# Kernel tuning notes

Hardware: AMD Instinct MI355X
Metric: run time of the kernel (lower is better)

## Reference

```python
import jax, jax.numpy as jnp
import numpy as np

S = 3072        # total tokens (3 images x 1024 patches)
E = 1280        # n_embed
H = 16          # n_heads
HD = E // H     # head_dim = 80
NSEG = 3


def rotate_half(x):
    x1 = x[..., : x.shape[-1] // 2]
    x2 = x[..., x.shape[-1] // 2 :]
    return jnp.concatenate((-x2, x1), axis=-1)


def setup_inputs() -> dict:
    key = jax.random.key(0)
    ks = jax.random.split(key, 6)
    x = jax.random.normal(ks[0], (S, E), dtype=jnp.float32)
    rotary_pos_emb = jax.random.normal(ks[1], (S, HD // 2), dtype=jnp.float32)
    qkv_w = jax.random.normal(ks[2], (3 * E, E), dtype=jnp.float32) * 0.02
    qkv_b = jax.random.normal(ks[3], (3 * E,), dtype=jnp.float32) * 0.02
    proj_w = jax.random.normal(ks[4], (E, E), dtype=jnp.float32) * 0.02
    proj_b = jax.random.normal(ks[5], (E,), dtype=jnp.float32) * 0.02
    cu_seqlens = (jnp.arange(NSEG + 1, dtype=jnp.int32) * (S // NSEG))  # [0,1024,2048,3072]
    return {"x": x, "rotary_pos_emb": rotary_pos_emb, "qkv_w": qkv_w,
            "qkv_b": qkv_b, "proj_w": proj_w, "proj_b": proj_b,
            "cu_seqlens": cu_seqlens}


def reference(x, rotary_pos_emb, qkv_w, qkv_b, proj_w, proj_b, cu_seqlens):
    seq_len = x.shape[0]
    # qkv projection (torch Linear: x @ W.T + b)
    qkv = (x @ qkv_w.T + qkv_b).reshape(seq_len, 3, H, HD)
    q, k, v = qkv[:, 0], qkv[:, 1], qkv[:, 2]          # each [S, H, HD]

    # inline RoPE: cos/sin repeated over the two halves of head_dim
    cos = jnp.cos(rotary_pos_emb)
    sin = jnp.sin(rotary_pos_emb)
    cos = jnp.concatenate([cos, cos], axis=-1)[:, None, :]  # [S, 1, HD]
    sin = jnp.concatenate([sin, sin], axis=-1)[:, None, :]
    q = q * cos + rotate_half(q) * sin
    k = k * cos + rotate_half(k) * sin

    # block-diagonal segment mask from cu_seqlens
    seg = jnp.searchsorted(cu_seqlens, jnp.arange(seq_len), side="right")  # [S]
    mask = seg[:, None] == seg[None, :]                 # [S, S] bool

    scale = jnp.asarray(1.0 / np.sqrt(HD), dtype=q.dtype)
    scores = jnp.einsum("qhd,khd->hqk", q, k) * scale   # [H, S, S]
    scores = jnp.where(mask[None], scores, jnp.finfo(scores.dtype).min)
    attn = jax.nn.softmax(scores, axis=-1)
    out = jnp.einsum("hqk,khd->qhd", attn, v).reshape(seq_len, E)
    return out @ proj_w.T + proj_b
```

## Files before the change

kernel.cpp:

```cpp
#include <hip/hip_runtime.h>
#include <hip/hip_bf16.h>
#include <math.h>

#define SEQ   3072
#define EMB   1280
#define NHEAD 16
#define HDIM  80
#define QKVN  3840
#define NSEGS 3

typedef __attribute__((ext_vector_type(8))) short bf16x8;
typedef __attribute__((ext_vector_type(4))) short bf16x4;
typedef __attribute__((ext_vector_type(4))) float f32x4;

__device__ __forceinline__ short f2bf(float f) {
    __hip_bfloat16 h = __float2bfloat16(f);
    return *reinterpret_cast<short*>(&h);
}
__device__ __forceinline__ float bf2f(short s) {
    unsigned int u = ((unsigned int)(unsigned short)s) << 16;
    union { unsigned int u; float f; } c; c.u = u;
    return c.f;
}

__device__ __forceinline__ void gload_lds16(const void* g, void* l) {
    __builtin_amdgcn_global_load_lds(
        (const __attribute__((address_space(1))) unsigned int*)g,
        (__attribute__((address_space(3))) unsigned int*)l, 16, 0, 0);
}

__global__ __launch_bounds__(256)
void cvt_bf16_kernel(const float* __restrict__ in, short* __restrict__ out, int n8)
{
    int i = blockIdx.x * 256 + threadIdx.x;
    if (i >= n8) return;
    float4 a = *reinterpret_cast<const float4*>(&in[i*8]);
    float4 b = *reinterpret_cast<const float4*>(&in[i*8+4]);
    bf16x8 o;
    o[0]=f2bf(a.x); o[1]=f2bf(a.y); o[2]=f2bf(a.z); o[3]=f2bf(a.w);
    o[4]=f2bf(b.x); o[5]=f2bf(b.y); o[6]=f2bf(b.z); o[7]=f2bf(b.w);
    *reinterpret_cast<bf16x8*>(&out[i*8]) = o;
}

__device__ __forceinline__ void store_val(float v, float* p) { *p = v; }
__device__ __forceinline__ void store_val(float v, short* p) { *p = f2bf(v); }

template<typename OT>
__global__ __launch_bounds__(256)
void gemm_bf16_nt(const short* __restrict__ A, int lda,
                  const short* __restrict__ B,
                  const float* __restrict__ bias, OT* __restrict__ C,
                  int M, int N, int K)
{
    __shared__ short As[128][32];
    __shared__ short Bs[128][32];

    const int tid = threadIdx.x;
    const int w   = tid >> 6;
    const int l   = tid & 63;
    const int l15 = l & 15;
    const int l4  = l >> 4;
    const int wr  = w >> 1;
    const int wc  = w & 1;
    const int row0 = blockIdx.y * 128;
    const int col0 = blockIdx.x * 128;

    const int srow = l >> 2;
    const int sk   = (l & 3) * 8;

    f32x4 acc[4][4];
    #pragma unroll
    for (int mi = 0; mi < 4; ++mi)
        #pragma unroll
        for (int ni = 0; ni < 4; ++ni) acc[mi][ni] = (f32x4){0.f,0.f,0.f,0.f};

    for (int k0 = 0; k0 < K; k0 += 32) {
        {
            const int c0 = w, c1 = w + 4;
            gload_lds16(&A[(size_t)(row0 + c0*16 + srow) * lda + k0 + sk], &As[c0*16][0]);
            gload_lds16(&A[(size_t)(row0 + c1*16 + srow) * lda + k0 + sk], &As[c1*16][0]);
            gload_lds16(&B[(size_t)(col0 + c0*16 + srow) * K   + k0 + sk], &Bs[c0*16][0]);
            gload_lds16(&B[(size_t)(col0 + c1*16 + srow) * K   + k0 + sk], &Bs[c1*16][0]);
        }
        __syncthreads();

        bf16x8 af[4], bfr[4];
        #pragma unroll
        for (int mi = 0; mi < 4; ++mi)
            af[mi] = *reinterpret_cast<const bf16x8*>(&As[wr*64 + mi*16 + l15][l4*8]);
        #pragma unroll
        for (int ni = 0; ni < 4; ++ni)
            bfr[ni] = *reinterpret_cast<const bf16x8*>(&Bs[wc*64 + ni*16 + l15][l4*8]);

        #pragma unroll
        for (int mi = 0; mi < 4; ++mi)
            #pragma unroll
            for (int ni = 0; ni < 4; ++ni)
                acc[mi][ni] = __builtin_amdgcn_mfma_f32_16x16x32_bf16(
                    af[mi], bfr[ni], acc[mi][ni], 0, 0, 0);
        __syncthreads();
    }

    #pragma unroll
    for (int ni = 0; ni < 4; ++ni) {
        int col = col0 + wc*64 + ni*16 + l15;
        float bv = bias[col];
        #pragma unroll
        for (int mi = 0; mi < 4; ++mi) {
            #pragma unroll
            for (int r = 0; r < 4; ++r) {
                size_t row = (size_t)(row0 + wr*64 + mi*16 + l4*4 + r);
                store_val(acc[mi][ni][r] + bv, &C[row * (size_t)N + col]);
            }
        }
    }
}

__global__ __launch_bounds__(256)
void rope_bf16_kernel(short* __restrict__ qkv, const float* __restrict__ rpe)
{
    int idx = blockIdx.x * 256 + threadIdx.x;
    int blk = idx % 5;
    int h   = (idx / 5) % NHEAD;
    int s   = (idx / (5*NHEAD)) % SEQ;
    int t   = idx / (5*NHEAD*SEQ);
    int d0  = blk * 8;

    const float* rp = rpe + s*40 + d0;
    short* p = qkv + (size_t)s*QKVN + t*EMB + h*HDIM + d0;
    bf16x8 v0 = *reinterpret_cast<const bf16x8*>(p);
    bf16x8 v1 = *reinterpret_cast<const bf16x8*>(p + 40);
    bf16x8 o0, o1;
    #pragma unroll
    for (int j = 0; j < 8; ++j) {
        float ang = rp[j];
        float sn = sinf(ang), cs = cosf(ang);
        float a = bf2f(v0[j]), b = bf2f(v1[j]);
        o0[j] = f2bf(a*cs - b*sn);
        o1[j] = f2bf(b*cs + a*sn);
    }
    *reinterpret_cast<bf16x8*>(p)      = o0;
    *reinterpret_cast<bf16x8*>(p + 40) = o1;
}

__global__ __launch_bounds__(256)
void attn_mfma(const short* __restrict__ qkv, const int* __restrict__ cu,
               short* __restrict__ aout)
{
    const int h   = blockIdx.z;
    const int seg = blockIdx.y;
    const int qt  = blockIdx.x;
    const int s0 = cu[seg], s1 = cu[seg+1];

    const int tid = threadIdx.x;
    const int w   = tid >> 6;
    const int l   = tid & 63;
    const int l15 = l & 15;
    const int l4  = l >> 4;

    __shared__ short Kl[64][128];
    __shared__ short Vt[HDIM][64];

    const int q0 = s0 + qt*64 + w*16;

    bf16x8 bzero;
    #pragma unroll
    for (int j = 0; j < 8; ++j) bzero[j] = 0;

    bf16x8 qf[3];
    {
        const short* qp = qkv + (size_t)(q0 + l15) * QKVN + h*HDIM;
        qf[0] = *reinterpret_cast<const bf16x8*>(qp + l4*8);
        qf[1] = *reinterpret_cast<const bf16x8*>(qp + 32 + l4*8);
        qf[2] = (l4 < 2) ? *reinterpret_cast<const bf16x8*>(qp + 64 + l4*8) : bzero;
    }

    float m = -3.4e38f, lsum = 0.f;
    f32x4 O[5];
    #pragma unroll
    for (int dt = 0; dt < 5; ++dt) O[dt] = (f32x4){0.f,0.f,0.f,0.f};

    int kkey[3], ku[3];
    const short* kptr[3];
    short* klds[3];
    #pragma unroll
    for (int i = 0; i < 3; ++i) {
        int task = tid + i*256;
        kkey[i] = task / 12;
        ku[i]   = task - kkey[i]*12;
        kptr[i] = qkv + (size_t)(s0 + kkey[i])*QKVN + EMB + h*HDIM + ku[i]*8;
        klds[i] = &Kl[kkey[i]][(ku[i] ^ (kkey[i] & 7))*8];
    }

    const int u1  = ((l >> 2) & 3) | ((l >> 5) << 2);
    const int bs1 = ((l >> 4) & 1) * 4 + (l & 3);
    const int k2  = w*16 + l15;
    const int u2  = ((k2 >> 2) & 3) | ((k2 >> 5) << 2);
    const int bs2 = ((k2 >> 4) & 1) * 4 + (k2 & 3);
    const bool sec = (l < 16);

    const short* vp1 = qkv + (size_t)(s0 + l)  * QKVN + 2*EMB + h*HDIM + w*16;
    const short* vp2 = qkv + (size_t)(s0 + k2) * QKVN + 2*EMB + h*HDIM + 64;

    bf16x8 kreg[3];
    bf16x8 vregA, vregB, vregC, vregD;
    #pragma unroll
    for (int i = 0; i < 3; ++i)
        kreg[i] = (ku[i] < 10) ? *reinterpret_cast<const bf16x8*>(kptr[i]) : bzero;
    vregA = *reinterpret_cast<const bf16x8*>(vp1);
    vregB = *reinterpret_cast<const bf16x8*>(vp1 + 8);
    if (sec) {
        vregC = *reinterpret_cast<const bf16x8*>(vp2);
        vregD = *reinterpret_cast<const bf16x8*>(vp2 + 8);
    }

    const float scale2 = 0.1612982054f;
    const int nk = s1 - s0;
    const size_t step = (size_t)64 * QKVN;
    short* vt_flat = &Vt[0][0];

    for (int kc = 0; kc < nk; kc += 64) {
        __syncthreads();

        #pragma unroll
        for (int i = 0; i < 3; ++i)
            *reinterpret_cast<bf16x8*>(klds[i]) = kreg[i];
        {
            const int rb = w*16*64;
            #pragma unroll
            for (int i = 0; i < 8; ++i) {
                vt_flat[rb + i*64      + ((u1 ^ i)       & 7)*8 + bs1] = vregA[i];
                vt_flat[rb + (i+8)*64  + ((u1 ^ i)       & 7)*8 + bs1] = vregB[i];
            }
            if (sec) {
                #pragma unroll
                for (int i = 0; i < 8; ++i) {
                    vt_flat[(64+i)*64  + ((u2 ^ i)       & 7)*8 + bs2] = vregC[i];
                    vt_flat[(72+i)*64  + ((u2 ^ i)       & 7)*8 + bs2] = vregD[i];
                }
            }
        }

        if (kc + 64 < nk) {
            #pragma unroll
            for (int i = 0; i < 3; ++i) {
                kptr[i] += step;
                if (ku[i] < 10) kreg[i] = *reinterpret_cast<const bf16x8*>(kptr[i]);
            }
            vp1 += step; vp2 += step;
            vregA = *reinterpret_cast<const bf16x8*>(vp1);
            vregB = *reinterpret_cast<const bf16x8*>(vp1 + 8);
            if (sec) {
                vregC = *reinterpret_cast<const bf16x8*>(vp2);
                vregD = *reinterpret_cast<const bf16x8*>(vp2 + 8);
            }
        }
        __syncthreads();

        f32x4 S[4];
        __builtin_amdgcn_s_setprio(1);
        #pragma unroll
        for (int ct = 0; ct < 4; ++ct) {
            f32x4 acc = (f32x4){0.f,0.f,0.f,0.f};
            int key = ct*16 + l15;
            #pragma unroll
            for (int t = 0; t < 3; ++t) {
                int u = (4*t + l4) ^ (key & 7);
                bf16x8 a = *reinterpret_cast<const bf16x8*>(&Kl[key][u*8]);
                acc = __builtin_amdgcn_mfma_f32_16x16x32_bf16(a, qf[t], acc, 0, 0, 0);
            }
            S[ct] = acc;
        }
        __builtin_amdgcn_s_setprio(0);

        float mx = -3.4e38f;
        #pragma unroll
        for (int ct = 0; ct < 4; ++ct)
            #pragma unroll
            for (int r = 0; r < 4; ++r) {
                float v = S[ct][r] * scale2;
                S[ct][r] = v;
                mx = fmaxf(mx, v);
            }
        mx = fmaxf(mx, __shfl_xor(mx, 16));
        mx = fmaxf(mx, __shfl_xor(mx, 32));
        float mn   = fmaxf(m, mx);
        float corr = exp2f(m - mn);
        float p[4][4];
        float ps = 0.f;
        #pragma unroll
        for (int ct = 0; ct < 4; ++ct)
            #pragma unroll
            for (int r = 0; r < 4; ++r) {
                float e = exp2f(S[ct][r] - mn);
                p[ct][r] = e;
                ps += e;
            }
        ps += __shfl_xor(ps, 16);
        ps += __shfl_xor(ps, 32);
        lsum = lsum * corr + ps;
        m = mn;
        #pragma unroll
        for (int dt = 0; dt < 5; ++dt)
            #pragma unroll
            for (int r = 0; r < 4; ++r) O[dt][r] *= corr;

        #pragma unroll
        for (int s2 = 0; s2 < 2; ++s2) {
            bf16x8 pb;
            #pragma unroll
            for (int j = 0; j < 8; ++j)
                pb[j] = f2bf(p[2*s2 + (j>>2)][j & 3]);
            __builtin_amdgcn_s_setprio(1);
            #pragma unroll
            for (int dt = 0; dt < 5; ++dt) {
                int d = dt*16 + l15;
                bf16x8 va = *reinterpret_cast<const bf16x8*>(
                    &vt_flat[d*64 + (((4*s2 + l4) ^ (d & 7)) & 7)*8]);
                O[dt] = __builtin_amdgcn_mfma_f32_16x16x32_bf16(va, pb, O[dt], 0, 0, 0);
            }
            __builtin_amdgcn_s_setprio(0);
        }
    }

    float inv = 1.f / lsum;
    short* orow = aout + (size_t)(q0 + l15) * EMB + h*HDIM;
    #pragma unroll
    for (int dt = 0; dt < 5; ++dt) {
        bf16x4 o4;
        #pragma unroll
        for (int r = 0; r < 4; ++r) o4[r] = f2bf(O[dt][r] * inv);
        *reinterpret_cast<bf16x4*>(&orow[dt*16 + 4*l4]) = o4;
    }
}

extern "C" void kernel_launch(void* const* d_in, const int* in_sizes, int n_in,
                              void* d_out, int out_size, void* d_ws, size_t ws_size,
                              hipStream_t stream)
{
    const float* x      = (const float*)d_in[0];
    const float* rpe    = (const float*)d_in[1];
    const float* qkv_w  = (const float*)d_in[2];
    const float* qkv_b  = (const float*)d_in[3];
    const float* proj_w = (const float*)d_in[4];
    const float* proj_b = (const float*)d_in[5];
    const int*   cu     = (const int*)d_in[6];
    float* out = (float*)d_out;

    short* ws       = (short*)d_ws;
    short* qkv_bf   = ws;
    short* x_bf     = qkv_bf  + (size_t)SEQ * QKVN;
    short* qkvw_bf  = x_bf    + (size_t)SEQ * EMB;
    short* projw_bf = qkvw_bf + (size_t)QKVN * EMB;
    short* attn_bf  = projw_bf+ (size_t)EMB * EMB;

    dim3 blk(256);

    cvt_bf16_kernel<<<dim3(SEQ*EMB/8/256),  blk, 0, stream>>>(x,      x_bf,     SEQ*EMB/8);
    cvt_bf16_kernel<<<dim3(QKVN*EMB/8/256), blk, 0, stream>>>(qkv_w,  qkvw_bf,  QKVN*EMB/8);
    cvt_bf16_kernel<<<dim3(EMB*EMB/8/256),  blk, 0, stream>>>(proj_w, projw_bf, EMB*EMB/8);

    gemm_bf16_nt<short><<<dim3(QKVN/128, SEQ/128), blk, 0, stream>>>(
        x_bf, EMB, qkvw_bf, qkv_b, qkv_bf, SEQ, QKVN, EMB);

    rope_bf16_kernel<<<dim3(2*SEQ*NHEAD*5/256), blk, 0, stream>>>(qkv_bf, rpe);

    attn_mfma<<<dim3((SEQ/NSEGS)/64, NSEGS, NHEAD), blk, 0, stream>>>(
        qkv_bf, cu, attn_bf);

    gemm_bf16_nt<float><<<dim3(EMB/128, SEQ/128), blk, 0, stream>>>(
        attn_bf, EMB, projw_bf, proj_b, out, SEQ, EMB, EMB);
}
```

Before: 158.6 us.

## Double attention key tile to 128, add lazy softmax rescale, fuse conversion kernels

```diff
diff --git a/kernel.cpp b/kernel.cpp
--- a/kernel.cpp
+++ b/kernel.cpp
@@ -30,16 +30,21 @@
 }
 
 __global__ __launch_bounds__(256)
-void cvt_bf16_kernel(const float* __restrict__ in, short* __restrict__ out, int n8)
-{
-    int i = blockIdx.x * 256 + threadIdx.x;
-    if (i >= n8) return;
-    float4 a = *reinterpret_cast<const float4*>(&in[i*8]);
-    float4 b = *reinterpret_cast<const float4*>(&in[i*8+4]);
+void cvt3_kernel(const float* __restrict__ a, short* __restrict__ oa, int na8,
+                 const float* __restrict__ b, short* __restrict__ ob, int nb8,
+                 const float* __restrict__ c, short* __restrict__ oc, int nc8)
+{
+    int j = blockIdx.x * 256 + threadIdx.x;
+    const float* src; short* dst;
+    if (j < na8) { src = a; dst = oa; }
+    else if ((j -= na8) < nb8) { src = b; dst = ob; }
+    else { j -= nb8; src = c; dst = oc; }
+    float4 x = *reinterpret_cast<const float4*>(&src[j*8]);
+    float4 y = *reinterpret_cast<const float4*>(&src[j*8+4]);
     bf16x8 o;
-    o[0]=f2bf(a.x); o[1]=f2bf(a.y); o[2]=f2bf(a.z); o[3]=f2bf(a.w);
-    o[4]=f2bf(b.x); o[5]=f2bf(b.y); o[6]=f2bf(b.z); o[7]=f2bf(b.w);
-    *reinterpret_cast<bf16x8*>(&out[i*8]) = o;
+    o[0]=f2bf(x.x); o[1]=f2bf(x.y); o[2]=f2bf(x.z); o[3]=f2bf(x.w);
+    o[4]=f2bf(y.x); o[5]=f2bf(y.y); o[6]=f2bf(y.z); o[7]=f2bf(y.w);
+    *reinterpret_cast<bf16x8*>(&dst[j*8]) = o;
 }
 
 __device__ __forceinline__ void store_val(float v, float* p) { *p = v; }
@@ -158,8 +163,8 @@
     const int l15 = l & 15;
     const int l4  = l >> 4;
 
-    __shared__ short Kl[64][128];
-    __shared__ short Vt[HDIM][64];
+    __shared__ short Kl[128][128];
+    __shared__ short Vt[HDIM][128];
 
     const int q0 = s0 + qt*64 + w*16;
 
@@ -180,87 +185,67 @@
     #pragma unroll
     for (int dt = 0; dt < 5; ++dt) O[dt] = (f32x4){0.f,0.f,0.f,0.f};
 
-    int kkey[3], ku[3];
-    const short* kptr[3];
-    short* klds[3];
-    #pragma unroll
-    for (int i = 0; i < 3; ++i) {
+    int koff[6]; short* klds[6]; bool kreal[6];
+    #pragma unroll
+    for (int i = 0; i < 6; ++i) {
         int task = tid + i*256;
-        kkey[i] = task / 12;
-        ku[i]   = task - kkey[i]*12;
-        kptr[i] = qkv + (size_t)(s0 + kkey[i])*QKVN + EMB + h*HDIM + ku[i]*8;
-        klds[i] = &Kl[kkey[i]][(ku[i] ^ (kkey[i] & 7))*8];
-    }
-
-    const int u1  = ((l >> 2) & 3) | ((l >> 5) << 2);
-    const int bs1 = ((l >> 4) & 1) * 4 + (l & 3);
-    const int k2  = w*16 + l15;
-    const int u2  = ((k2 >> 2) & 3) | ((k2 >> 5) << 2);
-    const int bs2 = ((k2 >> 4) & 1) * 4 + (k2 & 3);
-    const bool sec = (l < 16);
-
-    const short* vp1 = qkv + (size_t)(s0 + l)  * QKVN + 2*EMB + h*HDIM + w*16;
-    const short* vp2 = qkv + (size_t)(s0 + k2) * QKVN + 2*EMB + h*HDIM + 64;
-
-    bf16x8 kreg[3];
-    bf16x8 vregA, vregB, vregC, vregD;
-    #pragma unroll
-    for (int i = 0; i < 3; ++i)
-        kreg[i] = (ku[i] < 10) ? *reinterpret_cast<const bf16x8*>(kptr[i]) : bzero;
-    vregA = *reinterpret_cast<const bf16x8*>(vp1);
-    vregB = *reinterpret_cast<const bf16x8*>(vp1 + 8);
-    if (sec) {
-        vregC = *reinterpret_cast<const bf16x8*>(vp2);
-        vregD = *reinterpret_cast<const bf16x8*>(vp2 + 8);
-    }
+        int key  = task / 12;
+        int u    = task - key*12;
+        kreal[i] = (u < 10);
+        koff[i]  = key*QKVN + u*8;
+        klds[i]  = &Kl[key][(u ^ (key & 7))*8];
+    }
+    const short* kbase = qkv + (size_t)s0*QKVN + EMB + h*HDIM;
+
+    const int vk   = tid & 127;
+    const int vd0  = (tid >> 7) * 40;
+    const int vu   = ((vk >> 2) & 3) | (((vk >> 5) & 3) << 2);
+    const int vpos = ((vk >> 4) & 1) * 4 + (vk & 3);
+    const short* vbase = qkv + (size_t)(s0 + vk)*QKVN + 2*EMB + h*HDIM + vd0;
+
+    bf16x8 kreg[6], vreg[5];
+    #pragma unroll
+    for (int i = 0; i < 6; ++i)
+        kreg[i] = kreal[i] ? *reinterpret_cast<const bf16x8*>(kbase + koff[i]) : bzero;
+    #pragma unroll
+    for (int i = 0; i < 5; ++i)
+        vreg[i] = *reinterpret_cast<const bf16x8*>(vbase + 8*i);
 
     const float scale2 = 0.1612982054f;
     const int nk = s1 - s0;
-    const size_t step = (size_t)64 * QKVN;
+    const size_t step = (size_t)128 * QKVN;
     short* vt_flat = &Vt[0][0];
 
-    for (int kc = 0; kc < nk; kc += 64) {
+    for (int kc = 0; kc < nk; kc += 128) {
         __syncthreads();
 
         #pragma unroll
-        for (int i = 0; i < 3; ++i)
+        for (int i = 0; i < 6; ++i)
             *reinterpret_cast<bf16x8*>(klds[i]) = kreg[i];
-        {
-            const int rb = w*16*64;
-            #pragma unroll
-            for (int i = 0; i < 8; ++i) {
-                vt_flat[rb + i*64      + ((u1 ^ i)       & 7)*8 + bs1] = vregA[i];
-                vt_flat[rb + (i+8)*64  + ((u1 ^ i)       & 7)*8 + bs1] = vregB[i];
-            }
-            if (sec) {
-                #pragma unroll
-                for (int i = 0; i < 8; ++i) {
-                    vt_flat[(64+i)*64  + ((u2 ^ i)       & 7)*8 + bs2] = vregC[i];
-                    vt_flat[(72+i)*64  + ((u2 ^ i)       & 7)*8 + bs2] = vregD[i];
-                }
-            }
-        }
-
-        if (kc + 64 < nk) {
-            #pragma unroll
-            for (int i = 0; i < 3; ++i) {
-                kptr[i] += step;
-                if (ku[i] < 10) kreg[i] = *reinterpret_cast<const bf16x8*>(kptr[i]);
-            }
-            vp1 += step; vp2 += step;
-            vregA = *reinterpret_cast<const bf16x8*>(vp1);
-            vregB = *reinterpret_cast<const bf16x8*>(vp1 + 8);
-            if (sec) {
-                vregC = *reinterpret_cast<const bf16x8*>(vp2);
-                vregD = *reinterpret_cast<const bf16x8*>(vp2 + 8);
-            }
+        #pragma unroll
+        for (int i = 0; i < 5; ++i) {
+            #pragma unroll
+            for (int e = 0; e < 8; ++e) {
+                int d = vd0 + 8*i + e;
+                vt_flat[d*128 + ((vu ^ (d & 7))*8) + vpos] = vreg[i][e];
+            }
+        }
+
+        if (kc + 128 < nk) {
+            kbase += step; vbase += step;
+            #pragma unroll
+            for (int i = 0; i < 6; ++i)
+                if (kreal[i]) kreg[i] = *reinterpret_cast<const bf16x8*>(kbase + koff[i]);
+            #pragma unroll
+            for (int i = 0; i < 5; ++i)
+                vreg[i] = *reinterpret_cast<const bf16x8*>(vbase + 8*i);
         }
         __syncthreads();
 
-        f32x4 S[4];
+        f32x4 S[8];
         __builtin_amdgcn_s_setprio(1);
         #pragma unroll
-        for (int ct = 0; ct < 4; ++ct) {
+        for (int ct = 0; ct < 8; ++ct) {
             f32x4 acc = (f32x4){0.f,0.f,0.f,0.f};
             int key = ct*16 + l15;
             #pragma unroll
@@ -275,7 +260,7 @@
 
         float mx = -3.4e38f;
         #pragma unroll
-        for (int ct = 0; ct < 4; ++ct)
+        for (int ct = 0; ct < 8; ++ct)
             #pragma unroll
             for (int r = 0; r < 4; ++r) {
                 float v = S[ct][r] * scale2;
@@ -284,39 +269,41 @@
             }
         mx = fmaxf(mx, __shfl_xor(mx, 16));
         mx = fmaxf(mx, __shfl_xor(mx, 32));
-        float mn   = fmaxf(m, mx);
-        float corr = exp2f(m - mn);
-        float p[4][4];
+        if (!__all(mx - m <= 8.f)) {
+            float mn   = fmaxf(m, mx);
+            float corr = exp2f(m - mn);
+            lsum *= corr;
+            #pragma unroll
+            for (int dt = 0; dt < 5; ++dt)
+                #pragma unroll
+                for (int r = 0; r < 4; ++r) O[dt][r] *= corr;
+            m = mn;
+        }
         float ps = 0.f;
         #pragma unroll
-        for (int ct = 0; ct < 4; ++ct)
+        for (int ct = 0; ct < 8; ++ct)
             #pragma unroll
             for (int r = 0; r < 4; ++r) {
-                float e = exp2f(S[ct][r] - mn);
-                p[ct][r] = e;
+                float e = exp2f(S[ct][r] - m);
+                S[ct][r] = e;
                 ps += e;
             }
         ps += __shfl_xor(ps, 16);
         ps += __shfl_xor(ps, 32);
-        lsum = lsum * corr + ps;
-        m = mn;
-        #pragma unroll
-        for (int dt = 0; dt < 5; ++dt)
-            #pragma unroll
-            for (int r = 0; r < 4; ++r) O[dt][r] *= corr;
-
-        #pragma unroll
-        for (int s2 = 0; s2 < 2; ++s2) {
+        lsum += ps;
+
+        #pragma unroll
+        for (int s2 = 0; s2 < 4; ++s2) {
             bf16x8 pb;
             #pragma unroll
             for (int j = 0; j < 8; ++j)
-                pb[j] = f2bf(p[2*s2 + (j>>2)][j & 3]);
+                pb[j] = f2bf(S[2*s2 + (j>>2)][j & 3]);
             __builtin_amdgcn_s_setprio(1);
             #pragma unroll
             for (int dt = 0; dt < 5; ++dt) {
                 int d = dt*16 + l15;
                 bf16x8 va = *reinterpret_cast<const bf16x8*>(
-                    &vt_flat[d*64 + (((4*s2 + l4) ^ (d & 7)) & 7)*8]);
+                    &vt_flat[d*128 + (((4*s2 + l4) ^ (d & 7))*8)]);
                 O[dt] = __builtin_amdgcn_mfma_f32_16x16x32_bf16(va, pb, O[dt], 0, 0, 0);
             }
             __builtin_amdgcn_s_setprio(0);
@@ -356,9 +343,9 @@
 
     dim3 blk(256);
 
-    cvt_bf16_kernel<<<dim3(SEQ*EMB/8/256),  blk, 0, stream>>>(x,      x_bf,     SEQ*EMB/8);
-    cvt_bf16_kernel<<<dim3(QKVN*EMB/8/256), blk, 0, stream>>>(qkv_w,  qkvw_bf,  QKVN*EMB/8);
-    cvt_bf16_kernel<<<dim3(EMB*EMB/8/256),  blk, 0, stream>>>(proj_w, projw_bf, EMB*EMB/8);
+    const int na8 = SEQ*EMB/8, nb8 = QKVN*EMB/8, nc8 = EMB*EMB/8;
+    cvt3_kernel<<<dim3((na8+nb8+nc8)/256), blk, 0, stream>>>(
+        x, x_bf, na8, qkv_w, qkvw_bf, nb8, proj_w, projw_bf, nc8);
 
     gemm_bf16_nt<short><<<dim3(QKVN/128, SEQ/128), blk, 0, stream>>>(
         x_bf, EMB, qkvw_bf, qkv_b, qkv_bf, SEQ, QKVN, EMB);
```

Measured after the change: 174.1 us. +9.8%, slower.
